# Kernel tuning notes

Hardware: AMD Instinct MI355X
Metric: run time of the kernel (lower is better)

Reference implementation:

```python
import jax, jax.numpy as jnp
import numpy as np

N_EMB = 1024
N_HEAD = 16
HD = N_EMB // N_HEAD
ROPE_BASE = 10000.0


def _rope_cos_sin(seq_len, dim, dtype):
    inv_freq = 1.0 / (ROPE_BASE ** (jnp.arange(0, dim, 2, dtype=jnp.float32) / dim))
    t = jnp.arange(seq_len, dtype=jnp.float32)
    freqs = jnp.outer(t, inv_freq)              # [S, dim/2]
    emb = jnp.concatenate([freqs, freqs], -1)    # [S, dim]
    return jnp.cos(emb).astype(dtype), jnp.sin(emb).astype(dtype)


def _rotate_half(x):
    x1, x2 = jnp.split(x, 2, axis=-1)
    return jnp.concatenate([-x2, x1], axis=-1)


def _apply_rope(x):
    # x: [B, H, L, hd]; rotary over sequence axis (-2)
    cos, sin = _rope_cos_sin(x.shape[-2], x.shape[-1], x.dtype)
    return x * cos + _rotate_half(x) * sin


def setup_inputs() -> dict:
    key = jax.random.key(0)
    ks = jax.random.split(key, 8)
    B, T, S = 2, 2048, 2048
    std = 0.02
    return {
        "x": jax.random.normal(ks[0], (B, T, N_EMB), jnp.float32),
        "memory": jax.random.normal(ks[1], (B, S, N_EMB), jnp.float32),
        "q_w": jax.random.normal(ks[2], (N_EMB, N_EMB), jnp.float32) * std,
        "q_b": jnp.zeros((N_EMB,), jnp.float32),
        "kv_w": jax.random.normal(ks[3], (N_EMB, 2 * N_EMB), jnp.float32) * std,
        "kv_b": jnp.zeros((2 * N_EMB,), jnp.float32),
        "proj_w": jax.random.normal(ks[4], (N_EMB, N_EMB), jnp.float32) * std,
        "proj_b": jnp.zeros((N_EMB,), jnp.float32),
    }


def reference(x, memory, q_w, q_b, kv_w, kv_b, proj_w, proj_b):
    B, S, C = memory.shape
    T = x.shape[1]
    kv = memory @ kv_w + kv_b                      # [B,S,2C]
    K, V = jnp.split(kv, 2, axis=-1)
    Q = x @ q_w + q_b                              # [B,T,C]

    def heads(t, L):
        return t.reshape(B, L, N_HEAD, HD).transpose(0, 2, 1, 3)

    Q, K, V = heads(Q, T), heads(K, S), heads(V, S)
    Q = jax.nn.elu(Q) + 1.0                        # positive feature map
    K = jax.nn.elu(K) + 1.0
    Q_rot = _apply_rope(Q)
    K_rot = _apply_rope(K)
    # denom row-sum: sum_s Q.K_s == Q . (sum_s K_s) -- identical math, no SxT matrix
    denom = jnp.einsum('bhtd,bhd->bht', Q, K.sum(axis=2))[..., None]  # [B,H,T,1]
    att = jnp.einsum('bhtd,bhsd->bhts', Q_rot, K_rot) / denom          # [B,H,T,S]
    y = jnp.einsum('bhts,bhsd->bhtd', att, V)                          # [B,H,T,hd]
    y = y.transpose(0, 2, 1, 3).reshape(B, T, C)
    return y @ proj_w + proj_b
```

## Files before the change

kernel.cpp:

```cpp
#include <hip/hip_runtime.h>
#include <cstddef>
#include <cstdint>

#define B_SZ  2
#define T_SEQ 2048
#define S_SEQ 2048
#define C_EMB 1024
#define NH    16
#define HD    64
#define KDIM  1024

typedef __attribute__((ext_vector_type(8))) short bf16x8;
typedef __attribute__((ext_vector_type(4))) float f32x4;

#define OFF_XH    ((size_t)0)
#define OFF_XL    ((size_t)2097152)
#define OFF_MEMH  ((size_t)4194304)
#define OFF_MEML  ((size_t)6291456)
#define OFF_QWH   ((size_t)8388608)
#define OFF_QWL   ((size_t)8912896)
#define OFF_KVWH  ((size_t)9437184)
#define OFF_KVWL  ((size_t)10485760)
#define OFF_PWH   ((size_t)11534336)
#define OFF_PWL   ((size_t)12058624)
#define OFF_KSUM  ((size_t)12582912)
#define OFF_MT    ((size_t)12584960)
#define OFF_TAB   ((size_t)12716032)
#define OFF_YH    ((size_t)12847104)
#define OFF_YL    ((size_t)14944256)
#define WS_FLOATS ((size_t)17041408)

__device__ __forceinline__ float elu1(float v) {
    return v > 0.0f ? v + 1.0f : __expf(v);
}
__device__ __forceinline__ unsigned short bf16_rne(float x) {
    union { float f; unsigned int u; } v; v.f = x;
    unsigned int u = v.u;
    return (unsigned short)((u + 0x7FFFu + ((u >> 16) & 1u)) >> 16);
}
__device__ __forceinline__ float bf16_to_f(unsigned short h) {
    union { unsigned int u; float f; } v; v.u = ((unsigned int)h) << 16;
    return v.f;
}

#define PREP_BLOCKS 13064

__device__ __forceinline__ void split4_body(
    const float4* __restrict__ in, ushort4* __restrict__ hi,
    ushort4* __restrict__ lo, int i)
{
    float4 v = in[i];
    ushort4 h, l;
    h.x = bf16_rne(v.x); l.x = bf16_rne(v.x - bf16_to_f(h.x));
    h.y = bf16_rne(v.y); l.y = bf16_rne(v.y - bf16_to_f(h.y));
    h.z = bf16_rne(v.z); l.z = bf16_rne(v.z - bf16_to_f(h.z));
    h.w = bf16_rne(v.w); l.w = bf16_rne(v.w - bf16_to_f(h.w));
    hi[i] = h; lo[i] = l;
}

__device__ __forceinline__ void transpose_body(
    const float* __restrict__ W, unsigned short* __restrict__ Wth,
    unsigned short* __restrict__ Wtl, int K, int N, int bx, int by,
    float (*tile)[33])
{
    const int k0 = by * 32, n0 = bx * 32;
    const int tx = threadIdx.x & 31, ty = threadIdx.x >> 5;
    #pragma unroll
    for (int j = 0; j < 4; ++j)
        tile[ty + j * 8][tx] = W[(size_t)(k0 + ty + j * 8) * N + n0 + tx];
    __syncthreads();
    #pragma unroll
    for (int j = 0; j < 4; ++j) {
        float x = tile[tx][ty + j * 8];
        unsigned short h = bf16_rne(x);
        unsigned short l = bf16_rne(x - bf16_to_f(h));
        size_t o = (size_t)(n0 + ty + j * 8) * K + k0 + tx;
        Wth[o] = h; Wtl[o] = l;
    }
}

__global__ __launch_bounds__(256) void prep_kernel(
    const float* __restrict__ x, const float* __restrict__ memory,
    const float* __restrict__ q_w, const float* __restrict__ kv_w,
    const float* __restrict__ proj_w,
    unsigned short* __restrict__ xh, unsigned short* __restrict__ xl,
    unsigned short* __restrict__ mh, unsigned short* __restrict__ ml,
    unsigned short* __restrict__ qwh, unsigned short* __restrict__ qwl,
    unsigned short* __restrict__ kvwh, unsigned short* __restrict__ kvwl,
    unsigned short* __restrict__ pwh, unsigned short* __restrict__ pwl,
    float2* __restrict__ tab, float* __restrict__ zero_base)
{
    __shared__ float tile[32][33];
    const int bid = blockIdx.x;
    const int tid = threadIdx.x;
    if (bid < 4096) {
        split4_body((const float4*)x, (ushort4*)xh, (ushort4*)xl, bid * 256 + tid);
    } else if (bid < 8192) {
        split4_body((const float4*)memory, (ushort4*)mh, (ushort4*)ml, (bid - 4096) * 256 + tid);
    } else if (bid < 9216) {
        int i = bid - 8192;
        transpose_body(q_w, qwh, qwl, 1024, 1024, i & 31, i >> 5, tile);
    } else if (bid < 11264) {
        int i = bid - 9216;
        transpose_body(kv_w, kvwh, kvwl, 1024, 2048, i & 63, i >> 6, tile);
    } else if (bid < 12288) {
        int i = bid - 11264;
        transpose_body(proj_w, pwh, pwl, 1024, 1024, i & 31, i >> 5, tile);
    } else if (bid < 12544) {
        int idx = (bid - 12288) * 256 + tid;
        int pos = idx >> 5, i = idx & 31;
        double invf = exp(-(double)i * (9.210340371976184 / 32.0));
        float arg = (float)((double)pos * invf);
        float sn, cs;
        sincosf(arg, &sn, &cs);
        tab[idx] = make_float2(cs, sn);
    } else {
        int idx = (bid - 12544) * 256 + tid;
        if (idx < 2048 + 131072) zero_base[idx] = 0.0f;
    }
}

__device__ __forceinline__ void gemm_main_loop(
    const unsigned short* __restrict__ Ah, const unsigned short* __restrict__ Al,
    const unsigned short* __restrict__ Bth, const unsigned short* __restrict__ Btl,
    unsigned short* lds, int m0, int n0, f32x4 acc[4][4])
{
    const int tid = threadIdx.x;
    const int w = tid >> 6, lane = tid & 63;
    const int wr = w >> 1, wc = w & 1;
    const int quad = lane >> 4, lrow = lane & 15;

    const unsigned short* src = (w == 0) ? Ah : (w == 1) ? Al : (w == 2) ? Bth : Btl;
    const int rbase = (w < 2) ? m0 : n0;
    const int srow = lane >> 2;
    const int scol = (lane & 3) * 8;
    const unsigned short* gsrc = src + (size_t)(rbase + srow) * KDIM + scol;
    unsigned short* lbase = &lds[w * 4096];

    const unsigned short* As_h = lds;
    const unsigned short* As_l = lds + 4096;
    const unsigned short* Bs_h = lds + 8192;
    const unsigned short* Bs_l = lds + 12288;

    for (int k0 = 0; k0 < KDIM; k0 += 32) {
        #pragma unroll
        for (int i = 0; i < 8; ++i) {
            __builtin_amdgcn_global_load_lds(
                (const __attribute__((address_space(1))) unsigned int*)(gsrc + (size_t)i * 16 * KDIM + k0),
                (__attribute__((address_space(3))) unsigned int*)(lbase + i * 512),
                16, 0, 0);
        }
        __syncthreads();

        bf16x8 bh[4], bl[4];
        #pragma unroll
        for (int jt = 0; jt < 4; ++jt) {
            int nl = wc * 64 + jt * 16 + lrow;
            bh[jt] = *(const bf16x8*)&Bs_h[nl * 32 + quad * 8];
            bl[jt] = *(const bf16x8*)&Bs_l[nl * 32 + quad * 8];
        }
        #pragma unroll
        for (int it = 0; it < 4; ++it) {
            int ml = wr * 64 + it * 16 + lrow;
            bf16x8 ah = *(const bf16x8*)&As_h[ml * 32 + quad * 8];
            bf16x8 al = *(const bf16x8*)&As_l[ml * 32 + quad * 8];
            #pragma unroll
            for (int jt = 0; jt < 4; ++jt) {
                acc[it][jt] = __builtin_amdgcn_mfma_f32_16x16x32_bf16(ah, bh[jt], acc[it][jt], 0, 0, 0);
                acc[it][jt] = __builtin_amdgcn_mfma_f32_16x16x32_bf16(ah, bl[jt], acc[it][jt], 0, 0, 0);
                acc[it][jt] = __builtin_amdgcn_mfma_f32_16x16x32_bf16(al, bh[jt], acc[it][jt], 0, 0, 0);
            }
        }
        __syncthreads();
    }
}

__global__ __launch_bounds__(256) void gemm_kv(
    const unsigned short* __restrict__ Ah, const unsigned short* __restrict__ Al,
    const unsigned short* __restrict__ Bth, const unsigned short* __restrict__ Btl,
    const float* __restrict__ bias, const float2* __restrict__ tab,
    float* __restrict__ Ksum, float* __restrict__ Mt)
{
    __shared__ unsigned short smem[34816];
    const int tid = threadIdx.x;
    const int w = tid >> 6, lane = tid & 63;
    const int wr = w >> 1, wc = w & 1;
    const int quad = lane >> 4, lrow = lane & 15;
    const int h  = blockIdx.x;
    const int m0 = blockIdx.y * 128;
    const int b  = m0 >> 11;
    const int tbase = (m0 & 2047) + wr * 64;

    {
        const unsigned short* src = (w == 0) ? Ah : (w == 1) ? Al : (w == 2) ? Bth : Btl;
        const int srow = lane >> 2, scol = (lane & 3) * 8;
        const size_t rowbase = (w < 2) ? (size_t)(m0 + srow) : (size_t)(h * 64 + srow);
        const unsigned short* gsrc = src + rowbase * KDIM + scol;
        const size_t vskip = (w >= 2) ? (size_t)960 * KDIM : 0;
        unsigned short* lbase = &smem[w * 4096];
        const unsigned short* As_h = smem;
        const unsigned short* As_l = smem + 4096;
        const unsigned short* Bs_h = smem + 8192;
        const unsigned short* Bs_l = smem + 12288;

        f32x4 acc[4][4] = {};
        for (int k0 = 0; k0 < KDIM; k0 += 32) {
            #pragma unroll
            for (int i = 0; i < 8; ++i) {
                size_t goff = (size_t)i * 16 * KDIM + k0 + ((i >= 4) ? vskip : 0);
                __builtin_amdgcn_global_load_lds(
                    (const __attribute__((address_space(1))) unsigned int*)(gsrc + goff),
                    (__attribute__((address_space(3))) unsigned int*)(lbase + i * 512),
                    16, 0, 0);
            }
            __syncthreads();
            bf16x8 bh[4], bl[4];
            #pragma unroll
            for (int jt = 0; jt < 4; ++jt) {
                int nl = wc * 64 + jt * 16 + lrow;
                bh[jt] = *(const bf16x8*)&Bs_h[nl * 32 + quad * 8];
                bl[jt] = *(const bf16x8*)&Bs_l[nl * 32 + quad * 8];
            }
            #pragma unroll
            for (int it = 0; it < 4; ++it) {
                int ml = wr * 64 + it * 16 + lrow;
                bf16x8 ah = *(const bf16x8*)&As_h[ml * 32 + quad * 8];
                bf16x8 al = *(const bf16x8*)&As_l[ml * 32 + quad * 8];
                #pragma unroll
                for (int jt = 0; jt < 4; ++jt) {
                    acc[it][jt] = __builtin_amdgcn_mfma_f32_16x16x32_bf16(ah, bh[jt], acc[it][jt], 0, 0, 0);
                    acc[it][jt] = __builtin_amdgcn_mfma_f32_16x16x32_bf16(ah, bl[jt], acc[it][jt], 0, 0, 0);
                    acc[it][jt] = __builtin_amdgcn_mfma_f32_16x16x32_bf16(al, bh[jt], acc[it][jt], 0, 0, 0);
                }
            }
            __syncthreads();
        }

        const bool isK = (wc == 0);
        const int colg = (isK ? 0 : C_EMB) + h * 64;
        float bb[4];
        #pragma unroll
        for (int jt = 0; jt < 4; ++jt) bb[jt] = bias[colg + jt * 16 + lrow];
        #pragma unroll
        for (int it = 0; it < 4; ++it)
            #pragma unroll
            for (int jt = 0; jt < 4; ++jt)
                #pragma unroll
                for (int r = 0; r < 4; ++r) {
                    float v = acc[it][jt][r] + bb[jt];
                    acc[it][jt][r] = isK ? elu1(v) : v;
                }

        if (isK) {
            #pragma unroll
            for (int jt = 0; jt < 4; ++jt) {
                float p = 0.0f;
                #pragma unroll
                for (int it = 0; it < 4; ++it)
                    #pragma unroll
                    for (int r = 0; r < 4; ++r) p += acc[it][jt][r];
                p += __shfl_xor(p, 16);
                p += __shfl_xor(p, 32);
                if (quad == 0)
                    atomicAdd(&Ksum[b * C_EMB + h * 64 + jt * 16 + lrow], p);
            }
            #pragma unroll
            for (int it = 0; it < 4; ++it)
                #pragma unroll
                for (int r = 0; r < 4; ++r) {
                    int s = tbase + it * 16 + quad * 4 + r;
                    float2 c0 = tab[s * 32 + lrow];
                    float2 c1 = tab[s * 32 + 16 + lrow];
                    float a0 = acc[it][0][r], a1 = acc[it][1][r];
                    float a2 = acc[it][2][r], a3 = acc[it][3][r];
                    acc[it][0][r] = a0 * c0.x - a2 * c0.y;
                    acc[it][2][r] = a2 * c0.x + a0 * c0.y;
                    acc[it][1][r] = a1 * c1.x - a3 * c1.y;
                    acc[it][3][r] = a3 * c1.x + a1 * c1.y;
                }
        }

        unsigned short* Hd = smem + (isK ? 0 : 17408);
        unsigned short* Ld = Hd + 8704;
        #pragma unroll
        for (int jt = 0; jt < 4; ++jt) {
            int d = jt * 16 + lrow;
            #pragma unroll
            for (int it = 0; it < 4; ++it) {
                int t0loc = wr * 64 + it * 16 + quad * 4;
                ushort4 h4, l4;
                float v0 = acc[it][jt][0], v1 = acc[it][jt][1];
                float v2 = acc[it][jt][2], v3 = acc[it][jt][3];
                h4.x = bf16_rne(v0); l4.x = bf16_rne(v0 - bf16_to_f(h4.x));
                h4.y = bf16_rne(v1); l4.y = bf16_rne(v1 - bf16_to_f(h4.y));
                h4.z = bf16_rne(v2); l4.z = bf16_rne(v2 - bf16_to_f(h4.z));
                h4.w = bf16_rne(v3); l4.w = bf16_rne(v3 - bf16_to_f(h4.w));
                *(ushort4*)&Hd[d * 136 + t0loc] = h4;
                *(ushort4*)&Ld[d * 136 + t0loc] = l4;
            }
        }
    }
    __syncthreads();

    {
        const unsigned short* KH = smem;
        const unsigned short* KL = smem + 8704;
        const unsigned short* VH = smem + 17408;
        const unsigned short* VL = smem + 26112;
        const int mrow = w * 16 + lrow;
        f32x4 macc[4] = {};
        #pragma unroll
        for (int ks = 0; ks < 4; ++ks) {
            int kof = ks * 32 + quad * 8;
            bf16x8 vah = *(const bf16x8*)&VH[mrow * 136 + kof];
            bf16x8 val = *(const bf16x8*)&VL[mrow * 136 + kof];
            #pragma unroll
            for (int jt = 0; jt < 4; ++jt) {
                int nrow = jt * 16 + lrow;
                bf16x8 kbh = *(const bf16x8*)&KH[nrow * 136 + kof];
                bf16x8 kbl = *(const bf16x8*)&KL[nrow * 136 + kof];
                macc[jt] = __builtin_amdgcn_mfma_f32_16x16x32_bf16(vah, kbh, macc[jt], 0, 0, 0);
                macc[jt] = __builtin_amdgcn_mfma_f32_16x16x32_bf16(vah, kbl, macc[jt], 0, 0, 0);
                macc[jt] = __builtin_amdgcn_mfma_f32_16x16x32_bf16(val, kbh, macc[jt], 0, 0, 0);
            }
        }
        const int bh = b * NH + h;
        #pragma unroll
        for (int jt = 0; jt < 4; ++jt)
            #pragma unroll
            for (int r = 0; r < 4; ++r)
                atomicAdd(&Mt[((size_t)bh * 64 + w * 16 + quad * 4 + r) * 64 + jt * 16 + lrow],
                          macc[jt][r]);
    }
}

__global__ __launch_bounds__(256) void gemm_q(
    const unsigned short* __restrict__ Ah, const unsigned short* __restrict__ Al,
    const unsigned short* __restrict__ Bth, const unsigned short* __restrict__ Btl,
    const float* __restrict__ bias, const float2* __restrict__ tab,
    const float* __restrict__ Ksum, const float* __restrict__ Mt,
    unsigned short* __restrict__ Yh, unsigned short* __restrict__ Yl)
{
    __shared__ unsigned short smem[36864];
    const int m0 = blockIdx.y * 128, n0 = blockIdx.x * 128;
    f32x4 acc[4][4] = {};
    gemm_main_loop(Ah, Al, Bth, Btl, smem, m0, n0, acc);

    const int tid = threadIdx.x;
    const int w = tid >> 6, lane = tid & 63;
    const int wr = w >> 1, wc = w & 1;
    const int quad = lane >> 4, lrow = lane & 15;
    const int h = blockIdx.x * 2 + wc;
    const int b = m0 >> 11;
    const int tbase = (m0 & 2047) + wr * 64;
    const int bh = b * NH + h;

    float bb[4];
    #pragma unroll
    for (int jt = 0; jt < 4; ++jt) bb[jt] = bias[h * 64 + jt * 16 + lrow];
    #pragma unroll
    for (int it = 0; it < 4; ++it)
        #pragma unroll
        for (int jt = 0; jt < 4; ++jt)
            #pragma unroll
            for (int r = 0; r < 4; ++r)
                acc[it][jt][r] = elu1(acc[it][jt][r] + bb[jt]);

    float ks[4], den_reg[4][4];
    #pragma unroll
    for (int jt = 0; jt < 4; ++jt) ks[jt] = Ksum[b * C_EMB + h * 64 + jt * 16 + lrow];
    #pragma unroll
    for (int it = 0; it < 4; ++it)
        #pragma unroll
        for (int r = 0; r < 4; ++r) {
            float p = acc[it][0][r] * ks[0] + acc[it][1][r] * ks[1]
                    + acc[it][2][r] * ks[2] + acc[it][3][r] * ks[3];
            p += __shfl_xor(p, 1);
            p += __shfl_xor(p, 2);
            p += __shfl_xor(p, 4);
            p += __shfl_xor(p, 8);
            den_reg[it][r] = p;
        }

    #pragma unroll
    for (int it = 0; it < 4; ++it)
        #pragma unroll
        for (int r = 0; r < 4; ++r) {
            int s = tbase + it * 16 + quad * 4 + r;
            float2 c0 = tab[s * 32 + lrow];
            float2 c1 = tab[s * 32 + 16 + lrow];
            float a0 = acc[it][0][r], a1 = acc[it][1][r];
            float a2 = acc[it][2][r], a3 = acc[it][3][r];
            acc[it][0][r] = a0 * c0.x - a2 * c0.y;
            acc[it][2][r] = a2 * c0.x + a0 * c0.y;
            acc[it][1][r] = a1 * c1.x - a3 * c1.y;
            acc[it][3][r] = a3 * c1.x + a1 * c1.y;
        }

    unsigned short* QH = smem + w * 9216;
    unsigned short* QL = QH + 4608;
    #pragma unroll
    for (int it = 0; it < 4; ++it)
        #pragma unroll
        for (int jt = 0; jt < 4; ++jt)
            #pragma unroll
            for (int r = 0; r < 4; ++r) {
                int tloc = it * 16 + quad * 4 + r;
                int d = jt * 16 + lrow;
                float v = acc[it][jt][r];
                unsigned short hh = bf16_rne(v);
                QH[tloc * 72 + d] = hh;
                QL[tloc * 72 + d] = bf16_rne(v - bf16_to_f(hh));
            }
    __syncthreads();

    f32x4 acc2[4][4] = {};
    #pragma unroll
    for (int kc = 0; kc < 2; ++kc) {
        bf16x8 mbh[4], mbl[4];
        #pragma unroll
        for (int jt2 = 0; jt2 < 4; ++jt2) {
            const float* mp = &Mt[((size_t)bh * 64 + jt2 * 16 + lrow) * 64 + kc * 32 + quad * 8];
            #pragma unroll
            for (int e = 0; e < 8; ++e) {
                float x = mp[e];
                unsigned short hh = bf16_rne(x);
                mbh[jt2][e] = (short)hh;
                mbl[jt2][e] = (short)bf16_rne(x - bf16_to_f(hh));
            }
        }
        #pragma unroll
        for (int it2 = 0; it2 < 4; ++it2) {
            int ro = (it2 * 16 + lrow) * 72 + kc * 32 + quad * 8;
            bf16x8 qh = *(const bf16x8*)&QH[ro];
            bf16x8 ql = *(const bf16x8*)&QL[ro];
            #pragma unroll
            for (int jt2 = 0; jt2 < 4; ++jt2) {
                acc2[it2][jt2] = __builtin_amdgcn_mfma_f32_16x16x32_bf16(qh, mbh[jt2], acc2[it2][jt2], 0, 0, 0);
                acc2[it2][jt2] = __builtin_amdgcn_mfma_f32_16x16x32_bf16(qh, mbl[jt2], acc2[it2][jt2], 0, 0, 0);
                acc2[it2][jt2] = __builtin_amdgcn_mfma_f32_16x16x32_bf16(ql, mbh[jt2], acc2[it2][jt2], 0, 0, 0);
            }
        }
    }

    #pragma unroll
    for (int it2 = 0; it2 < 4; ++it2)
        #pragma unroll
        for (int jt2 = 0; jt2 < 4; ++jt2)
            #pragma unroll
            for (int r = 0; r < 4; ++r) {
                float v = acc2[it2][jt2][r] / den_reg[it2][r];
                size_t o = ((size_t)(m0 + wr * 64 + it2 * 16 + quad * 4 + r)) * C_EMB
                         + h * 64 + jt2 * 16 + lrow;
                unsigned short hh = bf16_rne(v);
                Yh[o] = hh;
                Yl[o] = bf16_rne(v - bf16_to_f(hh));
            }
}

__global__ __launch_bounds__(256) void gemm_out(
    const unsigned short* __restrict__ Ah, const unsigned short* __restrict__ Al,
    const unsigned short* __restrict__ Bth, const unsigned short* __restrict__ Btl,
    const float* __restrict__ bias, float* __restrict__ out)
{
    __shared__ unsigned short lds[16384];
    const int m0 = blockIdx.y * 128, n0 = blockIdx.x * 128;
    f32x4 acc[4][4] = {};
    gemm_main_loop(Ah, Al, Bth, Btl, lds, m0, n0, acc);

    const int tid = threadIdx.x;
    const int w = tid >> 6, lane = tid & 63;
    const int wr = w >> 1, wc = w & 1;
    const int quad = lane >> 4, lrow = lane & 15;

    #pragma unroll
    for (int jt = 0; jt < 4; ++jt) {
        int gc = n0 + wc * 64 + jt * 16 + lrow;
        float bb = bias[gc];
        #pragma unroll
        for (int it = 0; it < 4; ++it) {
            int grb = m0 + wr * 64 + it * 16 + quad * 4;
            #pragma unroll
            for (int r = 0; r < 4; ++r)
                out[(size_t)(grb + r) * C_EMB + gc] = acc[it][jt][r] + bb;
        }
    }
}

extern "C" void kernel_launch(void* const* d_in, const int* in_sizes, int n_in,
                              void* d_out, int out_size, void* d_ws, size_t ws_size,
                              hipStream_t stream)
{
    const float* x      = (const float*)d_in[0];
    const float* memory = (const float*)d_in[1];
    const float* q_w    = (const float*)d_in[2];
    const float* q_b    = (const float*)d_in[3];
    const float* kv_w   = (const float*)d_in[4];
    const float* kv_b   = (const float*)d_in[5];
    const float* proj_w = (const float*)d_in[6];
    const float* proj_b = (const float*)d_in[7];

    if (ws_size < WS_FLOATS * sizeof(float)) return;

    float* ws = (float*)d_ws;
    unsigned short* xh   = (unsigned short*)(ws + OFF_XH);
    unsigned short* xl   = (unsigned short*)(ws + OFF_XL);
    unsigned short* mh   = (unsigned short*)(ws + OFF_MEMH);
    unsigned short* ml   = (unsigned short*)(ws + OFF_MEML);
    unsigned short* qwh  = (unsigned short*)(ws + OFF_QWH);
    unsigned short* qwl  = (unsigned short*)(ws + OFF_QWL);
    unsigned short* kvwh = (unsigned short*)(ws + OFF_KVWH);
    unsigned short* kvwl = (unsigned short*)(ws + OFF_KVWL);
    unsigned short* pwh  = (unsigned short*)(ws + OFF_PWH);
    unsigned short* pwl  = (unsigned short*)(ws + OFF_PWL);
    unsigned short* Yh   = (unsigned short*)(ws + OFF_YH);
    unsigned short* Yl   = (unsigned short*)(ws + OFF_YL);
    float*  Ksum = ws + OFF_KSUM;
    float*  Mm   = ws + OFF_MT;
    float2* tab  = (float2*)(ws + OFF_TAB);

    prep_kernel<<<PREP_BLOCKS, 256, 0, stream>>>(
        x, memory, q_w, kv_w, proj_w,
        xh, xl, mh, ml, qwh, qwl, kvwh, kvwl, pwh, pwl,
        tab, Ksum );

    gemm_kv<<<dim3(16, 32), 256, 0, stream>>>(mh, ml, kvwh, kvwl, kv_b, tab, Ksum, Mm);
    gemm_q<<<dim3(8, 32), 256, 0, stream>>>(xh, xl, qwh, qwl, q_b, tab, Ksum, Mm, Yh, Yl);
    gemm_out<<<dim3(8, 32), 256, 0, stream>>>(Yh, Yl, pwh, pwl, proj_b, (float*)d_out);
}
```

Measured before the change: 264.9 us.

## Use 2-wave 128x64 tiles for Q/out GEMMs and K=64 steps in KV GEMM

```diff
diff --git a/kernel.cpp b/kernel.cpp
--- a/kernel.cpp
+++ b/kernel.cpp
@@ -120,48 +120,52 @@
     }
 }
 
-__device__ __forceinline__ void gemm_main_loop(
+__device__ __forceinline__ void gemm_main_loop_2w(
     const unsigned short* __restrict__ Ah, const unsigned short* __restrict__ Al,
     const unsigned short* __restrict__ Bth, const unsigned short* __restrict__ Btl,
     unsigned short* lds, int m0, int n0, f32x4 acc[4][4])
 {
     const int tid = threadIdx.x;
     const int w = tid >> 6, lane = tid & 63;
-    const int wr = w >> 1, wc = w & 1;
     const int quad = lane >> 4, lrow = lane & 15;
-
-    const unsigned short* src = (w == 0) ? Ah : (w == 1) ? Al : (w == 2) ? Bth : Btl;
-    const int rbase = (w < 2) ? m0 : n0;
     const int srow = lane >> 2;
     const int scol = (lane & 3) * 8;
-    const unsigned short* gsrc = src + (size_t)(rbase + srow) * KDIM + scol;
-    unsigned short* lbase = &lds[w * 4096];
+
+    const unsigned short* gsrcA = ((w == 0) ? Ah : Al) + (size_t)(m0 + srow) * KDIM + scol;
+    const unsigned short* gsrcB = ((w == 0) ? Bth : Btl) + (size_t)(n0 + srow) * KDIM + scol;
+    unsigned short* lbaseA = &lds[w * 4096];
+    unsigned short* lbaseB = &lds[8192 + w * 2048];
 
     const unsigned short* As_h = lds;
     const unsigned short* As_l = lds + 4096;
     const unsigned short* Bs_h = lds + 8192;
-    const unsigned short* Bs_l = lds + 12288;
+    const unsigned short* Bs_l = lds + 10240;
 
     for (int k0 = 0; k0 < KDIM; k0 += 32) {
         #pragma unroll
-        for (int i = 0; i < 8; ++i) {
+        for (int i = 0; i < 8; ++i)
             __builtin_amdgcn_global_load_lds(
-                (const __attribute__((address_space(1))) unsigned int*)(gsrc + (size_t)i * 16 * KDIM + k0),
-                (__attribute__((address_space(3))) unsigned int*)(lbase + i * 512),
+                (const __attribute__((address_space(1))) unsigned int*)(gsrcA + (size_t)i * 16 * KDIM + k0),
+                (__attribute__((address_space(3))) unsigned int*)(lbaseA + i * 512),
                 16, 0, 0);
-        }
+        #pragma unroll
+        for (int i = 0; i < 4; ++i)
+            __builtin_amdgcn_global_load_lds(
+                (const __attribute__((address_space(1))) unsigned int*)(gsrcB + (size_t)i * 16 * KDIM + k0),
+                (__attribute__((address_space(3))) unsigned int*)(lbaseB + i * 512),
+                16, 0, 0);
         __syncthreads();
 
         bf16x8 bh[4], bl[4];
         #pragma unroll
         for (int jt = 0; jt < 4; ++jt) {
-            int nl = wc * 64 + jt * 16 + lrow;
+            int nl = jt * 16 + lrow;
             bh[jt] = *(const bf16x8*)&Bs_h[nl * 32 + quad * 8];
             bl[jt] = *(const bf16x8*)&Bs_l[nl * 32 + quad * 8];
         }
         #pragma unroll
         for (int it = 0; it < 4; ++it) {
-            int ml = wr * 64 + it * 16 + lrow;
+            int ml = w * 64 + it * 16 + lrow;
             bf16x8 ah = *(const bf16x8*)&As_h[ml * 32 + quad * 8];
             bf16x8 al = *(const bf16x8*)&As_l[ml * 32 + quad * 8];
             #pragma unroll
@@ -197,40 +201,45 @@
         const size_t rowbase = (w < 2) ? (size_t)(m0 + srow) : (size_t)(h * 64 + srow);
         const unsigned short* gsrc = src + rowbase * KDIM + scol;
         const size_t vskip = (w >= 2) ? (size_t)960 * KDIM : 0;
-        unsigned short* lbase = &smem[w * 4096];
+        unsigned short* lbase = &smem[w * 8192];
         const unsigned short* As_h = smem;
-        const unsigned short* As_l = smem + 4096;
-        const unsigned short* Bs_h = smem + 8192;
-        const unsigned short* Bs_l = smem + 12288;
+        const unsigned short* As_l = smem + 8192;
+        const unsigned short* Bs_h = smem + 16384;
+        const unsigned short* Bs_l = smem + 24576;
 
         f32x4 acc[4][4] = {};
-        for (int k0 = 0; k0 < KDIM; k0 += 32) {
-            #pragma unroll
-            for (int i = 0; i < 8; ++i) {
-                size_t goff = (size_t)i * 16 * KDIM + k0 + ((i >= 4) ? vskip : 0);
-                __builtin_amdgcn_global_load_lds(
-                    (const __attribute__((address_space(1))) unsigned int*)(gsrc + goff),
-                    (__attribute__((address_space(3))) unsigned int*)(lbase + i * 512),
-                    16, 0, 0);
-            }
+        for (int k0 = 0; k0 < KDIM; k0 += 64) {
+            #pragma unroll
+            for (int p = 0; p < 2; ++p)
+                #pragma unroll
+                for (int i = 0; i < 8; ++i) {
+                    size_t goff = (size_t)i * 16 * KDIM + k0 + p * 32 + ((i >= 4) ? vskip : 0);
+                    __builtin_amdgcn_global_load_lds(
+                        (const __attribute__((address_space(1))) unsigned int*)(gsrc + goff),
+                        (__attribute__((address_space(3))) unsigned int*)(lbase + p * 4096 + i * 512),
+                        16, 0, 0);
+                }
             __syncthreads();
-            bf16x8 bh[4], bl[4];
-            #pragma unroll
-            for (int jt = 0; jt < 4; ++jt) {
-                int nl = wc * 64 + jt * 16 + lrow;
-                bh[jt] = *(const bf16x8*)&Bs_h[nl * 32 + quad * 8];
-                bl[jt] = *(const bf16x8*)&Bs_l[nl * 32 + quad * 8];
-            }
-            #pragma unroll
-            for (int it = 0; it < 4; ++it) {
-                int ml = wr * 64 + it * 16 + lrow;
-                bf16x8 ah = *(const bf16x8*)&As_h[ml * 32 + quad * 8];
-                bf16x8 al = *(const bf16x8*)&As_l[ml * 32 + quad * 8];
+            #pragma unroll
+            for (int p = 0; p < 2; ++p) {
+                bf16x8 bh[4], bl[4];
                 #pragma unroll
                 for (int jt = 0; jt < 4; ++jt) {
-                    acc[it][jt] = __builtin_amdgcn_mfma_f32_16x16x32_bf16(ah, bh[jt], acc[it][jt], 0, 0, 0);
-                    acc[it][jt] = __builtin_amdgcn_mfma_f32_16x16x32_bf16(ah, bl[jt], acc[it][jt], 0, 0, 0);
-                    acc[it][jt] = __builtin_amdgcn_mfma_f32_16x16x32_bf16(al, bh[jt], acc[it][jt], 0, 0, 0);
+                    int nl = wc * 64 + jt * 16 + lrow;
+                    bh[jt] = *(const bf16x8*)&Bs_h[p * 4096 + nl * 32 + quad * 8];
+                    bl[jt] = *(const bf16x8*)&Bs_l[p * 4096 + nl * 32 + quad * 8];
+                }
+                #pragma unroll
+                for (int it = 0; it < 4; ++it) {
+                    int ml = wr * 64 + it * 16 + lrow;
+                    bf16x8 ah = *(const bf16x8*)&As_h[p * 4096 + ml * 32 + quad * 8];
+                    bf16x8 al = *(const bf16x8*)&As_l[p * 4096 + ml * 32 + quad * 8];
+                    #pragma unroll
+                    for (int jt = 0; jt < 4; ++jt) {
+                        acc[it][jt] = __builtin_amdgcn_mfma_f32_16x16x32_bf16(ah, bh[jt], acc[it][jt], 0, 0, 0);
+                        acc[it][jt] = __builtin_amdgcn_mfma_f32_16x16x32_bf16(ah, bl[jt], acc[it][jt], 0, 0, 0);
+                        acc[it][jt] = __builtin_amdgcn_mfma_f32_16x16x32_bf16(al, bh[jt], acc[it][jt], 0, 0, 0);
+                    }
                 }
             }
             __syncthreads();
@@ -334,25 +343,24 @@
     }
 }
 
-__global__ __launch_bounds__(256) void gemm_q(
+__global__ __launch_bounds__(128) void gemm_q(
     const unsigned short* __restrict__ Ah, const unsigned short* __restrict__ Al,
     const unsigned short* __restrict__ Bth, const unsigned short* __restrict__ Btl,
     const float* __restrict__ bias, const float2* __restrict__ tab,
     const float* __restrict__ Ksum, const float* __restrict__ Mt,
     unsigned short* __restrict__ Yh, unsigned short* __restrict__ Yl)
 {
-    __shared__ unsigned short smem[36864];
-    const int m0 = blockIdx.y * 128, n0 = blockIdx.x * 128;
+    __shared__ unsigned short smem[18432];
+    const int h  = blockIdx.x;
+    const int m0 = blockIdx.y * 128;
     f32x4 acc[4][4] = {};
-    gemm_main_loop(Ah, Al, Bth, Btl, smem, m0, n0, acc);
+    gemm_main_loop_2w(Ah, Al, Bth, Btl, smem, m0, h * 64, acc);
 
     const int tid = threadIdx.x;
     const int w = tid >> 6, lane = tid & 63;
-    const int wr = w >> 1, wc = w & 1;
     const int quad = lane >> 4, lrow = lane & 15;
-    const int h = blockIdx.x * 2 + wc;
     const int b = m0 >> 11;
-    const int tbase = (m0 & 2047) + wr * 64;
+    const int tbase = (m0 & 2047) + w * 64;
     const int bh = b * NH + h;
 
     float bb[4];
@@ -412,7 +420,6 @@
                 QH[tloc * 72 + d] = hh;
                 QL[tloc * 72 + d] = bf16_rne(v - bf16_to_f(hh));
             }
-    __syncthreads();
 
     f32x4 acc2[4][4] = {};
     #pragma unroll
@@ -450,7 +457,7 @@
             #pragma unroll
             for (int r = 0; r < 4; ++r) {
                 float v = acc2[it2][jt2][r] / den_reg[it2][r];
-                size_t o = ((size_t)(m0 + wr * 64 + it2 * 16 + quad * 4 + r)) * C_EMB
+                size_t o = ((size_t)(m0 + w * 64 + it2 * 16 + quad * 4 + r)) * C_EMB
                          + h * 64 + jt2 * 16 + lrow;
                 unsigned short hh = bf16_rne(v);
                 Yh[o] = hh;
@@ -458,28 +465,27 @@
             }
 }
 
-__global__ __launch_bounds__(256) void gemm_out(
+__global__ __launch_bounds__(128) void gemm_out(
     const unsigned short* __restrict__ Ah, const unsigned short* __restrict__ Al,
     const unsigned short* __restrict__ Bth, const unsigned short* __restrict__ Btl,
     const float* __restrict__ bias, float* __restrict__ out)
 {
-    __shared__ unsigned short lds[16384];
-    const int m0 = blockIdx.y * 128, n0 = blockIdx.x * 128;
+    __shared__ unsigned short lds[12288];
+    const int m0 = blockIdx.y * 128, n0 = blockIdx.x * 64;
     f32x4 acc[4][4] = {};
-    gemm_main_loop(Ah, Al, Bth, Btl, lds, m0, n0, acc);
+    gemm_main_loop_2w(Ah, Al, Bth, Btl, lds, m0, n0, acc);
 
     const int tid = threadIdx.x;
     const int w = tid >> 6, lane = tid & 63;
-    const int wr = w >> 1, wc = w & 1;
     const int quad = lane >> 4, lrow = lane & 15;
 
     #pragma unroll
     for (int jt = 0; jt < 4; ++jt) {
-        int gc = n0 + wc * 64 + jt * 16 + lrow;
+        int gc = n0 + jt * 16 + lrow;
         float bb = bias[gc];
         #pragma unroll
         for (int it = 0; it < 4; ++it) {
-            int grb = m0 + wr * 64 + it * 16 + quad * 4;
+            int grb = m0 + w * 64 + it * 16 + quad * 4;
             #pragma unroll
             for (int r = 0; r < 4; ++r)
                 out[(size_t)(grb + r) * C_EMB + gc] = acc[it][jt][r] + bb;
@@ -525,6 +531,6 @@
         tab, Ksum );
 
     gemm_kv<<<dim3(16, 32), 256, 0, stream>>>(mh, ml, kvwh, kvwl, kv_b, tab, Ksum, Mm);
-    gemm_q<<<dim3(8, 32), 256, 0, stream>>>(xh, xl, qwh, qwl, q_b, tab, Ksum, Mm, Yh, Yl);
-    gemm_out<<<dim3(8, 32), 256, 0, stream>>>(Yh, Yl, pwh, pwl, proj_b, (float*)d_out);
-}
+    gemm_q<<<dim3(16, 32), 128, 0, stream>>>(xh, xl, qwh, qwl, q_b, tab, Ksum, Mm, Yh, Yl);
+    gemm_out<<<dim3(16, 32), 128, 0, stream>>>(Yh, Yl, pwh, pwl, proj_b, (float*)d_out);
+}
```

New measurement: 271.3 us. 2.4% more time.
